# Kernel tuning notes

Measured on AMD Instinct MI355X. Metric: run time of the kernel, lower is better.

The kernel has to match this reference:

```python
import jax, jax.numpy as jnp
import numpy as np

B, S, D = 4, 1024, 1024
H, DH = 16, 64
F = 4 * D
EPS = 1e-6


def _ln(x, scale, bias, axes=-1):
    mean = jnp.mean(x, axis=axes, keepdims=True)
    var = jnp.var(x, axis=axes, keepdims=True)
    return (x - mean) * jax.lax.rsqrt(var + EPS) * scale + bias


def setup_inputs() -> dict:
    key = jax.random.key(0)
    ks = jax.random.split(key, 20)
    sd = 1.0 / np.sqrt(D)
    sf = 1.0 / np.sqrt(F)
    inp = {
        'x': jax.random.normal(ks[0], (B, S, D), jnp.float32),
        'z': jax.random.normal(ks[1], (B, S, D), jnp.float32),
        'ln1_s': jnp.ones((D,), jnp.float32),
        'ln1_b': jnp.zeros((D,), jnp.float32),
        'Wq': jax.random.normal(ks[2], (D, D), jnp.float32) * sd,
        'bq': jnp.zeros((D,), jnp.float32),
        'Wk': jax.random.normal(ks[3], (D, D), jnp.float32) * sd,
        'bk': jnp.zeros((D,), jnp.float32),
        'Wv': jax.random.normal(ks[4], (D, D), jnp.float32) * sd,
        'bv': jnp.zeros((D,), jnp.float32),
        'qn_s': jnp.ones((H, DH), jnp.float32),
        'qn_b': jnp.zeros((H, DH), jnp.float32),
        'kn_s': jnp.ones((H, DH), jnp.float32),
        'kn_b': jnp.zeros((H, DH), jnp.float32),
        'Wo': jax.random.normal(ks[5], (D, D), jnp.float32) * sd,
        'bo': jnp.zeros((D,), jnp.float32),
        'ln2_s': jnp.ones((D,), jnp.float32),
        'ln2_b': jnp.zeros((D,), jnp.float32),
        'W1': jax.random.normal(ks[6], (D, F), jnp.float32) * sd,
        'b1': jnp.zeros((F,), jnp.float32),
        'W2': jax.random.normal(ks[7], (D, F), jnp.float32) * sd,
        'b2': jnp.zeros((F,), jnp.float32),
        'W3': jax.random.normal(ks[8], (F, D), jnp.float32) * sf,
        'b3': jnp.zeros((D,), jnp.float32),
    }
    return inp


def reference(x, z, ln1_s, ln1_b, Wq, bq, Wk, bk, Wv, bv, qn_s, qn_b, kn_s, kn_b,
              Wo, bo, ln2_s, ln2_b, W1, b1, W2, b2, W3, b3):
    # z is unused by the original module body
    x_skip = x
    xn = _ln(x, ln1_s, ln1_b)
    q = (xn @ Wq + bq).reshape(B, S, H, DH)
    k = (xn @ Wk + bk).reshape(B, S, H, DH)
    v = (xn @ Wv + bv).reshape(B, S, H, DH)
    # QK-norm: flax LayerNorm(feature_axes=(-2,-1)) still reduces over axis -1,
    # but carries (H, DH)-shaped scale/bias
    q = _ln(q, qn_s, qn_b)
    k = _ln(k, kn_s, kn_b)
    attn = jnp.einsum('bqhd,bkhd->bhqk', q, k) / jnp.sqrt(jnp.asarray(DH, q.dtype))
    attn = jax.nn.softmax(attn, axis=-1)
    out = jnp.einsum('bhqk,bkhd->bqhd', attn, v).reshape(B, S, D)
    x = x_skip + out @ Wo + bo
    x_skip = x
    xn = _ln(x, ln2_s, ln2_b)
    x1 = xn @ W1 + b1
    x2 = xn @ W2 + b2
    h = x1 * jax.nn.gelu(x2, approximate=True)  # GeGLU
    x = x_skip + h @ W3 + b3
    return x
```

## Files before the change

kernel.cpp:

```cpp
#include <hip/hip_runtime.h>

typedef unsigned short u16;
typedef __bf16  bfrag  __attribute__((ext_vector_type(8)));
typedef float   f32x4  __attribute__((ext_vector_type(4)));
typedef u16     u16x8  __attribute__((ext_vector_type(8)));
typedef u16     u16x4  __attribute__((ext_vector_type(4)));

__device__ __forceinline__ float bf2f(u16 u) {
    unsigned v = ((unsigned)u) << 16;
    return __builtin_bit_cast(float, v);
}
__device__ __forceinline__ u16 f2bf(float f) {
    unsigned x = __builtin_bit_cast(unsigned, f);
    unsigned r = (x + 0x7fffu + ((x >> 16) & 1u)) >> 16;
    return (u16)r;
}
__device__ __forceinline__ void g2l16(const u16* g, u16* l) {
    __builtin_amdgcn_global_load_lds((__attribute__((address_space(1))) void*)g,
                                     (__attribute__((address_space(3))) void*)l, 16, 0, 0);
}
__device__ __forceinline__ float gelu_tanh(float x) {
    float c = 1.5957691216057308f * (x + 0.044715f * x * x * x);
    return x * __frcp_rn(1.0f + __expf(-c));
}

#define SW64(l)   (((((l) & 7) ^ (((l) >> 3) & 7))) * 8)
#define RS64(kk, quad, l15)  (((((kk) * 4 + (quad)) ^ ((l15) & 7))) * 8)

__global__ __launch_bounds__(256) void wtln(
        const float* __restrict__ Wq, const float* __restrict__ Wk,
        const float* __restrict__ Wv, const float* __restrict__ Wo,
        const float* __restrict__ W1, const float* __restrict__ W2,
        const float* __restrict__ W3,
        u16* __restrict__ WqkvT, u16* __restrict__ WoT,
        u16* __restrict__ W12T, u16* __restrict__ W3T,
        const float* __restrict__ x, const float* __restrict__ ln1_s,
        const float* __restrict__ ln1_b, u16* __restrict__ xn1) {
    __shared__ float tile[32][33];
    int blk = blockIdx.x;
    if (blk >= 16384) {
        int row = blk - 16384, t = threadIdx.x;
        float4 v = ((const float4*)(x + (size_t)row * 1024))[t];
        float sum = v.x + v.y + v.z + v.w;
        float sq  = v.x * v.x + v.y * v.y + v.z * v.z + v.w * v.w;
#pragma unroll
        for (int off = 1; off < 64; off <<= 1) {
            sum += __shfl_xor(sum, off);
            sq  += __shfl_xor(sq,  off);
        }
        float* s1 = &tile[0][0];
        float* s2 = &tile[0][8];
        int wave = t >> 6;
        if ((t & 63) == 0) { s1[wave] = sum; s2[wave] = sq; }
        __syncthreads();
        sum = s1[0] + s1[1] + s1[2] + s1[3];
        sq  = s2[0] + s2[1] + s2[2] + s2[3];
        float mean = sum * (1.0f / 1024.0f);
        float var  = sq  * (1.0f / 1024.0f) - mean * mean;
        float inv  = rsqrtf(var + 1e-6f);
        float4 sc = ((const float4*)ln1_s)[t], bb = ((const float4*)ln1_b)[t];
        u16x4 o;
        o[0] = f2bf((v.x - mean) * inv * sc.x + bb.x);
        o[1] = f2bf((v.y - mean) * inv * sc.y + bb.y);
        o[2] = f2bf((v.z - mean) * inv * sc.z + bb.z);
        o[3] = f2bf((v.w - mean) * inv * sc.w + bb.w);
        *(u16x4*)&xn1[(size_t)row * 1024 + t * 4] = o;
        return;
    }
    const float* W; u16* Wt; int R, C, local;
    if (blk < 3072) {
        int w = blk >> 10; local = blk & 1023;
        W = (w == 0) ? Wq : (w == 1) ? Wk : Wv;
        Wt = WqkvT + (size_t)w * 1024 * 1024; R = 1024; C = 1024;
    } else if (blk < 4096) { W = Wo; Wt = WoT; R = 1024; C = 1024; local = blk - 3072; }
    else if (blk < 8192)   { W = W1; Wt = W12T; R = 1024; C = 4096; local = blk - 4096; }
    else if (blk < 12288)  { W = W2; Wt = W12T + (size_t)4096 * 1024; R = 1024; C = 4096; local = blk - 8192; }
    else                   { W = W3; Wt = W3T; R = 4096; C = 1024; local = blk - 12288; }
    int tiles_x = C >> 5;
    int c0 = (local % tiles_x) * 32, r0 = (local / tiles_x) * 32;
    int tx = threadIdx.x & 31, ty = threadIdx.x >> 5;
#pragma unroll
    for (int i = 0; i < 32; i += 8)
        tile[ty + i][tx] = W[(size_t)(r0 + ty + i) * C + c0 + tx];
    __syncthreads();
#pragma unroll
    for (int i = 0; i < 32; i += 8)
        Wt[(size_t)(c0 + ty + i) * R + r0 + tx] = f2bf(tile[tx][ty + i]);
}

template <int EPI>
__global__ __launch_bounds__(256, 3) void gemm64(const u16* __restrict__ A,
                                                 const u16* __restrict__ Bt,
                                                 const float* __restrict__ bias,
                                                 const float* __restrict__ bias2,
                                                 const float* __restrict__ bias3,
                                                 const float* __restrict__ qn_s,
                                                 const float* __restrict__ qn_b,
                                                 const float* __restrict__ kn_s,
                                                 const float* __restrict__ kn_b,
                                                 u16* __restrict__ o0,
                                                 u16* __restrict__ o1,
                                                 u16* __restrict__ o2,
                                                 u16* __restrict__ o3,
                                                 int M, int N, int K, int Klen) {
    __shared__ u16 As[128 * 64];
    __shared__ u16 Bs[128 * 64];
    int tid = threadIdx.x, wave = tid >> 6, lane = tid & 63;
    int quad = lane >> 4, l15 = lane & 15;
    int row0 = blockIdx.y * 128, col0 = blockIdx.x * 128;
    int kz = blockIdx.z;
    int wr = (wave >> 1) * 64, wc = (wave & 1) * 64;
    int swz = SW64(lane);

    f32x4 acc[4][4] = {};

    const u16* gA = A  + (size_t)(row0 + wave * 32 + (lane >> 3)) * K + kz * Klen + swz;
    const u16* gB = Bt + (size_t)(col0 + wave * 32 + (lane >> 3)) * K + kz * Klen + swz;
    u16* lA = &As[wave * 32 * 64];
    u16* lB = &Bs[wave * 32 * 64];

    for (int k0 = 0; k0 < Klen; k0 += 64) {
        __syncthreads();
#pragma unroll
        for (int j = 0; j < 4; j++) {
            g2l16(gA + k0 + j * 8 * K, lA + j * 8 * 64);
            g2l16(gB + k0 + j * 8 * K, lB + j * 8 * 64);
        }
        __syncthreads();
#pragma unroll
        for (int kk = 0; kk < 2; kk++) {
            int rs = RS64(kk, quad, l15);
            bfrag af[4], bf[4];
#pragma unroll
            for (int mi = 0; mi < 4; mi++)
                af[mi] = *(const bfrag*)&As[(wr + mi * 16 + l15) * 64 + rs];
#pragma unroll
            for (int ni = 0; ni < 4; ni++)
                bf[ni] = *(const bfrag*)&Bs[(wc + ni * 16 + l15) * 64 + rs];
#pragma unroll
            for (int mi = 0; mi < 4; mi++)
#pragma unroll
                for (int ni = 0; ni < 4; ni++)
                    acc[mi][ni] = __builtin_amdgcn_mfma_f32_16x16x32_bf16(
                        af[mi], bf[ni], acc[mi][ni], 0, 0, 0);
        }
    }

    if (EPI == 0) {
        u16* P = (kz == 0) ? o0 : (kz == 1) ? o1 : (kz == 2) ? o2 : o3;
#pragma unroll
        for (int mi = 0; mi < 4; mi++) {
            int rbase = row0 + wr + mi * 16 + quad * 4;
#pragma unroll
            for (int r = 0; r < 4; r++)
#pragma unroll
                for (int ni = 0; ni < 4; ni++)
                    P[(size_t)(rbase + r) * N + col0 + wc + ni * 16 + l15] =
                        f2bf(acc[mi][ni][r]);
        }
    } else {
        int cbase = col0 + wc;
        int z = cbase >> 10;
        int hd = (cbase >> 6) & 15;
        const float* bp = (z == 0) ? bias : (z == 1) ? bias2 : bias3;
        float post = (z == 0) ? 0.125f : 1.0f;
        float bv[4], sn[4], bn[4];
#pragma unroll
        for (int ni = 0; ni < 4; ni++)
            bv[ni] = bp[(cbase & 1023) + ni * 16 + l15];
        if (z < 2) {
            const float* ns = (z == 0) ? qn_s : kn_s;
            const float* nb = (z == 0) ? qn_b : kn_b;
#pragma unroll
            for (int ni = 0; ni < 4; ni++) {
                sn[ni] = ns[hd * 64 + ni * 16 + l15];
                bn[ni] = nb[hd * 64 + ni * 16 + l15];
            }
        }
#pragma unroll
        for (int mi = 0; mi < 4; mi++) {
            int rbase = row0 + wr + mi * 16 + quad * 4;
#pragma unroll
            for (int r = 0; r < 4; r++) {
                float v0 = acc[mi][0][r] + bv[0];
                float v1 = acc[mi][1][r] + bv[1];
                float v2 = acc[mi][2][r] + bv[2];
                float v3 = acc[mi][3][r] + bv[3];
                size_t rb = (size_t)(rbase + r) * N + cbase;
                if (z == 2) {
                    o0[rb + 0 * 16 + l15] = f2bf(v0);
                    o0[rb + 1 * 16 + l15] = f2bf(v1);
                    o0[rb + 2 * 16 + l15] = f2bf(v2);
                    o0[rb + 3 * 16 + l15] = f2bf(v3);
                } else {
                    float s  = v0 + v1 + v2 + v3;
                    float sq = v0 * v0 + v1 * v1 + v2 * v2 + v3 * v3;
#pragma unroll
                    for (int m = 1; m < 16; m <<= 1) {
                        s  += __shfl_xor(s,  m);
                        sq += __shfl_xor(sq, m);
                    }
                    float mean = s * (1.0f / 64.0f);
                    float var  = sq * (1.0f / 64.0f) - mean * mean;
                    float inv  = rsqrtf(var + 1e-6f);
                    o0[rb + 0 * 16 + l15] = f2bf(((v0 - mean) * inv * sn[0] + bn[0]) * post);
                    o0[rb + 1 * 16 + l15] = f2bf(((v1 - mean) * inv * sn[1] + bn[1]) * post);
                    o0[rb + 2 * 16 + l15] = f2bf(((v2 - mean) * inv * sn[2] + bn[2]) * post);
                    o0[rb + 3 * 16 + l15] = f2bf(((v3 - mean) * inv * sn[3] + bn[3]) * post);
                }
            }
        }
    }
}

__global__ __launch_bounds__(256, 2) void gemm_w12(const u16* __restrict__ A,
                                                   const u16* __restrict__ W12T,
                                                   const float* __restrict__ b1,
                                                   const float* __restrict__ b2,
                                                   u16* __restrict__ H) {
    __shared__ u16 As[128 * 64];
    __shared__ u16 B1s[128 * 64];
    __shared__ u16 B2s[128 * 64];
    int tid = threadIdx.x, wave = tid >> 6, lane = tid & 63;
    int quad = lane >> 4, l15 = lane & 15;
    int row0 = blockIdx.y * 128, col0 = blockIdx.x * 128;
    int wr = (wave >> 1) * 64, wc = (wave & 1) * 64;
    int swz = SW64(lane);

    f32x4 acc1[4][4] = {}, acc2[4][4] = {};

    const u16* gA  = A    + (size_t)(row0 + wave * 32 + (lane >> 3)) * 1024 + swz;
    const u16* gB1 = W12T + (size_t)(col0 + wave * 32 + (lane >> 3)) * 1024 + swz;
    const u16* gB2 = gB1  + (size_t)4096 * 1024;
    u16* lA  = &As [wave * 32 * 64];
    u16* lB1 = &B1s[wave * 32 * 64];
    u16* lB2 = &B2s[wave * 32 * 64];

    for (int k0 = 0; k0 < 1024; k0 += 64) {
        __syncthreads();
#pragma unroll
        for (int j = 0; j < 4; j++) {
            g2l16(gA  + k0 + j * 8 * 1024, lA  + j * 8 * 64);
            g2l16(gB1 + k0 + j * 8 * 1024, lB1 + j * 8 * 64);
            g2l16(gB2 + k0 + j * 8 * 1024, lB2 + j * 8 * 64);
        }
        __syncthreads();
#pragma unroll
        for (int kk = 0; kk < 2; kk++) {
            int rs = RS64(kk, quad, l15);
            bfrag af[4], b1f[4], b2f[4];
#pragma unroll
            for (int mi = 0; mi < 4; mi++)
                af[mi] = *(const bfrag*)&As[(wr + mi * 16 + l15) * 64 + rs];
#pragma unroll
            for (int ni = 0; ni < 4; ni++) {
                b1f[ni] = *(const bfrag*)&B1s[(wc + ni * 16 + l15) * 64 + rs];
                b2f[ni] = *(const bfrag*)&B2s[(wc + ni * 16 + l15) * 64 + rs];
            }
#pragma unroll
            for (int mi = 0; mi < 4; mi++)
#pragma unroll
                for (int ni = 0; ni < 4; ni++) {
                    acc1[mi][ni] = __builtin_amdgcn_mfma_f32_16x16x32_bf16(
                        af[mi], b1f[ni], acc1[mi][ni], 0, 0, 0);
                    acc2[mi][ni] = __builtin_amdgcn_mfma_f32_16x16x32_bf16(
                        af[mi], b2f[ni], acc2[mi][ni], 0, 0, 0);
                }
        }
    }

    float bv1[4], bv2[4];
    int cols[4];
#pragma unroll
    for (int ni = 0; ni < 4; ni++) {
        cols[ni] = col0 + wc + ni * 16 + l15;
        bv1[ni] = b1[cols[ni]];
        bv2[ni] = b2[cols[ni]];
    }
#pragma unroll
    for (int mi = 0; mi < 4; mi++) {
        int rbase = row0 + wr + mi * 16 + quad * 4;
#pragma unroll
        for (int r = 0; r < 4; r++) {
#pragma unroll
            for (int ni = 0; ni < 4; ni++) {
                float x1 = acc1[mi][ni][r] + bv1[ni];
                float x2 = acc2[mi][ni][r] + bv2[ni];
                H[(size_t)(rbase + r) * 4096 + cols[ni]] = f2bf(x1 * gelu_tanh(x2));
            }
        }
    }
}

__global__ __launch_bounds__(256) void reduce_ln(const u16* __restrict__ p0,
                                                 const u16* __restrict__ p1,
                                                 const float* __restrict__ x,
                                                 const float* __restrict__ bo,
                                                 const float* __restrict__ s,
                                                 const float* __restrict__ b,
                                                 float* __restrict__ xmid,
                                                 u16* __restrict__ xn2) {
    int row = blockIdx.x, t = threadIdx.x;
    size_t i = (size_t)row * 1024 + t * 4;
    float4 xv = *(const float4*)&x[i];
    float4 bb = *(const float4*)&bo[t * 4];
    u16x4 a0 = *(const u16x4*)&p0[i];
    u16x4 a1 = *(const u16x4*)&p1[i];
    float4 v;
    v.x = xv.x + bb.x + bf2f(a0[0]) + bf2f(a1[0]);
    v.y = xv.y + bb.y + bf2f(a0[1]) + bf2f(a1[1]);
    v.z = xv.z + bb.z + bf2f(a0[2]) + bf2f(a1[2]);
    v.w = xv.w + bb.w + bf2f(a0[3]) + bf2f(a1[3]);
    *(float4*)&xmid[i] = v;
    float sum = v.x + v.y + v.z + v.w;
    float sq  = v.x * v.x + v.y * v.y + v.z * v.z + v.w * v.w;
#pragma unroll
    for (int off = 1; off < 64; off <<= 1) {
        sum += __shfl_xor(sum, off);
        sq  += __shfl_xor(sq,  off);
    }
    __shared__ float s1[4], s2[4];
    int wave = t >> 6;
    if ((t & 63) == 0) { s1[wave] = sum; s2[wave] = sq; }
    __syncthreads();
    sum = s1[0] + s1[1] + s1[2] + s1[3];
    sq  = s2[0] + s2[1] + s2[2] + s2[3];
    float mean = sum * (1.0f / 1024.0f);
    float var  = sq  * (1.0f / 1024.0f) - mean * mean;
    float inv  = rsqrtf(var + 1e-6f);
    float4 sc = ((const float4*)s)[t], lb = ((const float4*)b)[t];
    u16x4 o;
    o[0] = f2bf((v.x - mean) * inv * sc.x + lb.x);
    o[1] = f2bf((v.y - mean) * inv * sc.y + lb.y);
    o[2] = f2bf((v.z - mean) * inv * sc.z + lb.z);
    o[3] = f2bf((v.w - mean) * inv * sc.w + lb.w);
    *(u16x4*)&xn2[i] = o;
}

__global__ __launch_bounds__(256) void reduce4(const u16* __restrict__ p0,
                                               const u16* __restrict__ p1,
                                               const u16* __restrict__ p2,
                                               const u16* __restrict__ p3,
                                               const float* __restrict__ xmid,
                                               const float* __restrict__ b3,
                                               float* __restrict__ out) {
    size_t i = ((size_t)blockIdx.x * 256 + threadIdx.x) * 4;
    float4 xm = *(const float4*)&xmid[i];
    float4 bb = *(const float4*)&b3[i & 1023];
    u16x4 a0 = *(const u16x4*)&p0[i];
    u16x4 a1 = *(const u16x4*)&p1[i];
    u16x4 a2 = *(const u16x4*)&p2[i];
    u16x4 a3 = *(const u16x4*)&p3[i];
    float4 o;
    o.x = xm.x + bb.x + bf2f(a0[0]) + bf2f(a1[0]) + bf2f(a2[0]) + bf2f(a3[0]);
    o.y = xm.y + bb.y + bf2f(a0[1]) + bf2f(a1[1]) + bf2f(a2[1]) + bf2f(a3[1]);
    o.z = xm.z + bb.z + bf2f(a0[2]) + bf2f(a1[2]) + bf2f(a2[2]) + bf2f(a3[2]);
    o.w = xm.w + bb.w + bf2f(a0[3]) + bf2f(a1[3]) + bf2f(a2[3]) + bf2f(a3[3]);
    *(float4*)&out[i] = o;
}

#define LPK 72
#define LPV 72
#define LPP 68
__global__ __launch_bounds__(256, 4) void flash(const u16* __restrict__ qkv,
                                                u16* __restrict__ o) {
    int qt = blockIdx.x, h = blockIdx.y, b = blockIdx.z;
    int tid = threadIdx.x, wave = tid >> 6, lane = tid & 63;
    int quad = lane >> 4, l15 = lane & 15;

    __shared__ u16 Ks[64 * LPK];
    __shared__ u16 Vt[64 * LPV];
    __shared__ u16 Ps[64 * LPP];

    const u16* qrow = qkv + (size_t)(b * 1024 + qt * 64 + wave * 16 + l15) * 3072
                      + h * 64 + quad * 8;
    bfrag aq0 = *(const bfrag*)qrow;
    bfrag aq1 = *(const bfrag*)(qrow + 32);

    f32x4 accO[4] = {};
    float l_run[4] = {0.f, 0.f, 0.f, 0.f};

    for (int kt = 0; kt < 16; kt++) {
        __syncthreads();
        {
            int row = tid >> 2, seg = tid & 3;
            const u16* ksrc = qkv + (size_t)(b * 1024 + kt * 64 + row) * 3072
                              + 1024 + h * 64 + seg * 16;
            *(u16x8*)&Ks[row * LPK + seg * 16]     = *(const u16x8*)ksrc;
            *(u16x8*)&Ks[row * LPK + seg * 16 + 8] = *(const u16x8*)(ksrc + 8);
        }
        {
            const u16* vsrc = qkv + (size_t)(b * 1024 + kt * 64 + lane) * 3072
                              + 2048 + h * 64 + wave * 16;
            u16x8 v0 = *(const u16x8*)vsrc, v1 = *(const u16x8*)(vsrc + 8);
#pragma unroll
            for (int j = 0; j < 8; j++) Vt[(wave * 16 + j) * LPV + lane]     = v0[j];
#pragma unroll
            for (int j = 0; j < 8; j++) Vt[(wave * 16 + 8 + j) * LPV + lane] = v1[j];
        }
        __syncthreads();

        f32x4 accS[4] = {};
#pragma unroll
        for (int ct = 0; ct < 4; ct++) {
            bfrag bk0 = *(const bfrag*)&Ks[(ct * 16 + l15) * LPK + quad * 8];
            bfrag bk1 = *(const bfrag*)&Ks[(ct * 16 + l15) * LPK + 32 + quad * 8];
            accS[ct] = __builtin_amdgcn_mfma_f32_16x16x32_bf16(aq0, bk0, accS[ct], 0, 0, 0);
            accS[ct] = __builtin_amdgcn_mfma_f32_16x16x32_bf16(aq1, bk1, accS[ct], 0, 0, 0);
        }

#pragma unroll
        for (int r = 0; r < 4; r++) {
            float p0 = __expf(accS[0][r]);
            float p1 = __expf(accS[1][r]);
            float p2 = __expf(accS[2][r]);
            float p3 = __expf(accS[3][r]);
            l_run[r] += (p0 + p1) + (p2 + p3);
            int pbase = (wave * 16 + quad * 4 + r) * LPP + l15;
            Ps[pbase + 0]  = f2bf(p0);
            Ps[pbase + 16] = f2bf(p1);
            Ps[pbase + 32] = f2bf(p2);
            Ps[pbase + 48] = f2bf(p3);
        }

#pragma unroll
        for (int kk = 0; kk < 2; kk++) {
            const u16* pp = &Ps[(wave * 16 + l15) * LPP + kk * 32 + quad * 8];
            u16x4 lo = *(const u16x4*)pp;
            u16x4 hi = *(const u16x4*)(pp + 4);
            u16x8 apu;
            apu[0] = lo[0]; apu[1] = lo[1]; apu[2] = lo[2]; apu[3] = lo[3];
            apu[4] = hi[0]; apu[5] = hi[1]; apu[6] = hi[2]; apu[7] = hi[3];
            bfrag ap = __builtin_bit_cast(bfrag, apu);
#pragma unroll
            for (int oc = 0; oc < 4; oc++) {
                bfrag bv = *(const bfrag*)&Vt[(oc * 16 + l15) * LPV + kk * 32 + quad * 8];
                accO[oc] = __builtin_amdgcn_mfma_f32_16x16x32_bf16(ap, bv, accO[oc], 0, 0, 0);
            }
        }
    }

#pragma unroll
    for (int r = 0; r < 4; r++) {
        float l = l_run[r];
#pragma unroll
        for (int m = 1; m < 16; m <<= 1) l += __shfl_xor(l, m);
        float linv = 1.0f / l;
        int srow = qt * 64 + wave * 16 + quad * 4 + r;
#pragma unroll
        for (int oc = 0; oc < 4; oc++)
            o[(size_t)(b * 1024 + srow) * 1024 + h * 64 + oc * 16 + l15] =
                f2bf(accO[oc][r] * linv);
    }
}

extern "C" void kernel_launch(void* const* d_in, const int* in_sizes, int n_in,
                              void* d_out, int out_size, void* d_ws, size_t ws_size,
                              hipStream_t stream) {
    const float* x     = (const float*)d_in[0];
    const float* ln1_s = (const float*)d_in[2];
    const float* ln1_b = (const float*)d_in[3];
    const float* Wq = (const float*)d_in[4];  const float* bq = (const float*)d_in[5];
    const float* Wk = (const float*)d_in[6];  const float* bk = (const float*)d_in[7];
    const float* Wv = (const float*)d_in[8];  const float* bv = (const float*)d_in[9];
    const float* qn_s = (const float*)d_in[10]; const float* qn_b = (const float*)d_in[11];
    const float* kn_s = (const float*)d_in[12]; const float* kn_b = (const float*)d_in[13];
    const float* Wo = (const float*)d_in[14]; const float* bo = (const float*)d_in[15];
    const float* ln2_s = (const float*)d_in[16]; const float* ln2_b = (const float*)d_in[17];
    const float* W1 = (const float*)d_in[18]; const float* b1 = (const float*)d_in[19];
    const float* W2 = (const float*)d_in[20]; const float* b2 = (const float*)d_in[21];
    const float* W3 = (const float*)d_in[22]; const float* b3 = (const float*)d_in[23];
    float* out = (float*)d_out;

    char* ws = (char*)d_ws;
    const size_t MB = (size_t)1 << 20;
    u16* WqkvT = (u16*)(ws + 0);
    u16* WoT   = (u16*)(ws + 6 * MB);
    u16* W12T  = (u16*)(ws + 8 * MB);
    u16* W3T   = (u16*)(ws + 24 * MB);
    u16* xn1   = (u16*)(ws + 32 * MB);
    u16* attn  = (u16*)(ws + 32 * MB);
    u16* xn2   = (u16*)(ws + 32 * MB);
    u16* qkv   = (u16*)(ws + 40 * MB);
    float* xmid = (float*)(ws + 40 * MB);
    u16* p3    = (u16*)(ws + 56 * MB);
    u16* h     = (u16*)(ws + 64 * MB);
    u16* wp0   = (u16*)(ws + 64 * MB);
    u16* wp1   = (u16*)(ws + 72 * MB);
    u16* p0    = (u16*)(ws + 0);
    u16* p1    = (u16*)(ws + 8 * MB);
    u16* p2    = (u16*)(ws + 16 * MB);

    wtln<<<20480, 256, 0, stream>>>(Wq, Wk, Wv, Wo, W1, W2, W3,
                                    WqkvT, WoT, W12T, W3T,
                                    x, ln1_s, ln1_b, xn1);

    gemm64<4><<<dim3(24, 32, 1), 256, 0, stream>>>(
        xn1, WqkvT, bq, bk, bv, qn_s, qn_b, kn_s, kn_b,
        qkv, nullptr, nullptr, nullptr, 4096, 3072, 1024, 1024);

    flash<<<dim3(16, 16, 4), 256, 0, stream>>>(qkv, attn);

    gemm64<0><<<dim3(8, 32, 2), 256, 0, stream>>>(
        attn, WoT, nullptr, nullptr, nullptr, nullptr, nullptr, nullptr, nullptr,
        wp0, wp1, nullptr, nullptr, 4096, 1024, 1024, 512);

    reduce_ln<<<4096, 256, 0, stream>>>(wp0, wp1, x, bo, ln2_s, ln2_b, xmid, xn2);

    gemm_w12<<<dim3(32, 32), 256, 0, stream>>>(xn2, W12T, b1, b2, h);

    gemm64<0><<<dim3(8, 32, 4), 256, 0, stream>>>(
        h, W3T, nullptr, nullptr, nullptr, nullptr, nullptr, nullptr, nullptr,
        p0, p1, p2, p3, 4096, 1024, 4096, 1024);

    reduce4<<<4096, 256, 0, stream>>>(p0, p1, p2, p3, xmid, b3, out);
}
```

Measured before the change: 404.7 us.

## Rewrite GeGLU W1/W2 GEMM as 256x256 8-wave double-buffered pipelined kernel

Weight transpose now interleaves W1 and W2 columns in 64-wide groups so one B tile holds matching x1/x2 columns. The GeGLU GEMM becomes a 512-thread kernel with 256x256 tiles and a two-buffer LDS pipeline in 128KB of dynamic shared memory. Its eight phases per K step each overlap global-to-LDS loads with MFMA work, using explicit barriers, vmcnt waits and setprio. The epilogue passes gelu values between paired waves through LDS to form x1*gelu(x2). This trades higher LDS use and lower occupancy for better data reuse and overlap, and relies on hand-written waitcnt logic that must stay correct.

```diff
diff --git a/kernel.cpp b/kernel.cpp
--- a/kernel.cpp
+++ b/kernel.cpp
@@ -67,14 +67,14 @@
         *(u16x4*)&xn1[(size_t)row * 1024 + t * 4] = o;
         return;
     }
-    const float* W; u16* Wt; int R, C, local;
+    const float* W; u16* Wt; int R, C, local; int ilv = -1;
     if (blk < 3072) {
         int w = blk >> 10; local = blk & 1023;
         W = (w == 0) ? Wq : (w == 1) ? Wk : Wv;
         Wt = WqkvT + (size_t)w * 1024 * 1024; R = 1024; C = 1024;
     } else if (blk < 4096) { W = Wo; Wt = WoT; R = 1024; C = 1024; local = blk - 3072; }
-    else if (blk < 8192)   { W = W1; Wt = W12T; R = 1024; C = 4096; local = blk - 4096; }
-    else if (blk < 12288)  { W = W2; Wt = W12T + (size_t)4096 * 1024; R = 1024; C = 4096; local = blk - 8192; }
+    else if (blk < 8192)   { W = W1; Wt = W12T; R = 1024; C = 4096; local = blk - 4096; ilv = 0; }
+    else if (blk < 12288)  { W = W2; Wt = W12T; R = 1024; C = 4096; local = blk - 8192; ilv = 1; }
     else                   { W = W3; Wt = W3T; R = 4096; C = 1024; local = blk - 12288; }
     int tiles_x = C >> 5;
     int c0 = (local % tiles_x) * 32, r0 = (local / tiles_x) * 32;
@@ -84,8 +84,11 @@
         tile[ty + i][tx] = W[(size_t)(r0 + ty + i) * C + c0 + tx];
     __syncthreads();
 #pragma unroll
-    for (int i = 0; i < 32; i += 8)
-        Wt[(size_t)(c0 + ty + i) * R + r0 + tx] = f2bf(tile[tx][ty + i]);
+    for (int i = 0; i < 32; i += 8) {
+        int c = c0 + ty + i;
+        int orow = (ilv < 0) ? c : ((c >> 6) * 128 + ilv * 64 + (c & 63));
+        Wt[(size_t)orow * R + r0 + tx] = f2bf(tile[tx][ty + i]);
+    }
 }
 
 template <int EPI>
@@ -213,80 +216,123 @@
     }
 }
 
-__global__ __launch_bounds__(256, 2) void gemm_w12(const u16* __restrict__ A,
-                                                   const u16* __restrict__ W12T,
-                                                   const float* __restrict__ b1,
-                                                   const float* __restrict__ b2,
-                                                   u16* __restrict__ H) {
-    __shared__ u16 As[128 * 64];
-    __shared__ u16 B1s[128 * 64];
-    __shared__ u16 B2s[128 * 64];
-    int tid = threadIdx.x, wave = tid >> 6, lane = tid & 63;
+#define PH8(BUFI, S, ISSUE, TAIL)                                              \
+  {                                                                            \
+    const u16* LA = sm + (BUFI) * 32768;                                       \
+    const u16* LB = LA + 16384;                                                \
+    if ((S) == 0) {                                                            \
+      _Pragma("unroll") for (int ni = 0; ni < 4; ++ni)                         \
+      _Pragma("unroll") for (int kk = 0; kk < 2; ++kk)                         \
+        bfr[ni][kk] = *(const bfrag*)&LB[(wcg + ni * 16 + l15) * 64            \
+                                         + RS64(kk, quad, l15)];               \
+    }                                                                          \
+    bfrag a00 = *(const bfrag*)&LA[(wr128 + ((S)*2)     * 16 + l15) * 64 + RS64(0, quad, l15)]; \
+    bfrag a01 = *(const bfrag*)&LA[(wr128 + ((S)*2)     * 16 + l15) * 64 + RS64(1, quad, l15)]; \
+    bfrag a10 = *(const bfrag*)&LA[(wr128 + ((S)*2 + 1) * 16 + l15) * 64 + RS64(0, quad, l15)]; \
+    bfrag a11 = *(const bfrag*)&LA[(wr128 + ((S)*2 + 1) * 16 + l15) * 64 + RS64(1, quad, l15)]; \
+    ISSUE;                                                                     \
+    asm volatile("" ::: "memory");                                             \
+    __builtin_amdgcn_s_barrier();                                              \
+    asm volatile("s_waitcnt lgkmcnt(0)" ::: "memory");                         \
+    __builtin_amdgcn_s_setprio(1);                                             \
+    _Pragma("unroll") for (int ni = 0; ni < 4; ++ni) {                         \
+      acc[(S)*2][ni]     = __builtin_amdgcn_mfma_f32_16x16x32_bf16(a00, bfr[ni][0], acc[(S)*2][ni], 0, 0, 0);         \
+      acc[(S)*2][ni]     = __builtin_amdgcn_mfma_f32_16x16x32_bf16(a01, bfr[ni][1], acc[(S)*2][ni], 0, 0, 0);         \
+      acc[(S)*2 + 1][ni] = __builtin_amdgcn_mfma_f32_16x16x32_bf16(a10, bfr[ni][0], acc[(S)*2 + 1][ni], 0, 0, 0);     \
+      acc[(S)*2 + 1][ni] = __builtin_amdgcn_mfma_f32_16x16x32_bf16(a11, bfr[ni][1], acc[(S)*2 + 1][ni], 0, 0, 0);     \
+    }                                                                          \
+    __builtin_amdgcn_s_setprio(0);                                             \
+    TAIL;                                                                      \
+    asm volatile("" ::: "memory");                                             \
+    __builtin_amdgcn_s_barrier();                                              \
+    asm volatile("" ::: "memory");                                             \
+  }
+
+__global__ __launch_bounds__(512, 2) void gemm_w12_8ph(
+        const u16* __restrict__ A, const u16* __restrict__ BI,
+        const float* __restrict__ b1, const float* __restrict__ b2,
+        u16* __restrict__ H) {
+    extern __shared__ __align__(16) u16 sm[];
+    int tid = threadIdx.x, w = tid >> 6, lane = tid & 63;
     int quad = lane >> 4, l15 = lane & 15;
-    int row0 = blockIdx.y * 128, col0 = blockIdx.x * 128;
-    int wr = (wave >> 1) * 64, wc = (wave & 1) * 64;
-    int swz = SW64(lane);
-
-    f32x4 acc1[4][4] = {}, acc2[4][4] = {};
-
-    const u16* gA  = A    + (size_t)(row0 + wave * 32 + (lane >> 3)) * 1024 + swz;
-    const u16* gB1 = W12T + (size_t)(col0 + wave * 32 + (lane >> 3)) * 1024 + swz;
-    const u16* gB2 = gB1  + (size_t)4096 * 1024;
-    u16* lA  = &As [wave * 32 * 64];
-    u16* lB1 = &B1s[wave * 32 * 64];
-    u16* lB2 = &B2s[wave * 32 * 64];
-
-    for (int k0 = 0; k0 < 1024; k0 += 64) {
-        __syncthreads();
-#pragma unroll
-        for (int j = 0; j < 4; j++) {
-            g2l16(gA  + k0 + j * 8 * 1024, lA  + j * 8 * 64);
-            g2l16(gB1 + k0 + j * 8 * 1024, lB1 + j * 8 * 64);
-            g2l16(gB2 + k0 + j * 8 * 1024, lB2 + j * 8 * 64);
-        }
-        __syncthreads();
-#pragma unroll
-        for (int kk = 0; kk < 2; kk++) {
-            int rs = RS64(kk, quad, l15);
-            bfrag af[4], b1f[4], b2f[4];
-#pragma unroll
-            for (int mi = 0; mi < 4; mi++)
-                af[mi] = *(const bfrag*)&As[(wr + mi * 16 + l15) * 64 + rs];
-#pragma unroll
-            for (int ni = 0; ni < 4; ni++) {
-                b1f[ni] = *(const bfrag*)&B1s[(wc + ni * 16 + l15) * 64 + rs];
-                b2f[ni] = *(const bfrag*)&B2s[(wc + ni * 16 + l15) * 64 + rs];
-            }
-#pragma unroll
-            for (int mi = 0; mi < 4; mi++)
-#pragma unroll
-                for (int ni = 0; ni < 4; ni++) {
-                    acc1[mi][ni] = __builtin_amdgcn_mfma_f32_16x16x32_bf16(
-                        af[mi], b1f[ni], acc1[mi][ni], 0, 0, 0);
-                    acc2[mi][ni] = __builtin_amdgcn_mfma_f32_16x16x32_bf16(
-                        af[mi], b2f[ni], acc2[mi][ni], 0, 0, 0);
-                }
-        }
-    }
-
-    float bv1[4], bv2[4];
-    int cols[4];
-#pragma unroll
-    for (int ni = 0; ni < 4; ni++) {
-        cols[ni] = col0 + wc + ni * 16 + l15;
-        bv1[ni] = b1[cols[ni]];
-        bv2[ni] = b2[cols[ni]];
-    }
-#pragma unroll
-    for (int mi = 0; mi < 4; mi++) {
-        int rbase = row0 + wr + mi * 16 + quad * 4;
-#pragma unroll
-        for (int r = 0; r < 4; r++) {
-#pragma unroll
-            for (int ni = 0; ni < 4; ni++) {
-                float x1 = acc1[mi][ni][r] + bv1[ni];
-                float x2 = acc2[mi][ni][r] + bv2[ni];
-                H[(size_t)(rbase + r) * 4096 + cols[ni]] = f2bf(x1 * gelu_tanh(x2));
+    int row0  = blockIdx.y * 256;
+    int nrow0 = blockIdx.x * 256;
+    int wr128 = (w >> 2) * 128, wcg = (w & 3) * 64;
+    int strow = w * 8 + (lane >> 3);
+    int swz8  = ((lane & 7) ^ ((lane >> 3) & 7)) * 8;
+    int lw8   = w * 8;
+
+    const u16* gA = A  + (size_t)(row0  + strow) * 1024 + swz8;
+    const u16* gB = BI + (size_t)(nrow0 + strow) * 1024 + swz8;
+
+    f32x4 acc[8][4] = {};
+    bfrag bfr[4][2];
+
+    auto stage = [&](int bufi, int isB, int half, int t) {
+        const u16* g = (isB ? gB : gA) + (size_t)half * 128 * 1024 + t * 64;
+        u16* l = sm + bufi * 32768 + isB * 16384 + (half * 128 + lw8) * 64;
+        g2l16(g, l);
+        g2l16(g + 64 * 1024, l + 64 * 64);
+    };
+
+    stage(0, 1, 0, 0); stage(0, 1, 1, 0);
+    stage(0, 0, 0, 0); stage(0, 0, 1, 0);
+    stage(1, 1, 0, 1); stage(1, 1, 1, 1);
+    asm volatile("s_waitcnt vmcnt(4)" ::: "memory");
+    __builtin_amdgcn_s_barrier();
+    asm volatile("" ::: "memory");
+
+#pragma unroll 1
+    for (int i = 0; i < 8; ++i) {
+        int t = 2 * i;
+        bool more = (i < 7);
+        PH8(0, 0, { stage(1, 0, 0, t + 1); }, {});
+        PH8(0, 1, { stage(1, 0, 1, t + 1); }, {});
+        PH8(0, 2, { if (more) stage(0, 1, 0, t + 2); }, {});
+        PH8(0, 3, { if (more) stage(0, 1, 1, t + 2); },
+                  { if (more) asm volatile("s_waitcnt vmcnt(4)" ::: "memory");
+                    else      asm volatile("s_waitcnt vmcnt(0)" ::: "memory"); });
+        PH8(1, 0, { if (more) stage(0, 0, 0, t + 2); }, {});
+        PH8(1, 1, { if (more) stage(0, 0, 1, t + 2); }, {});
+        PH8(1, 2, { if (more) stage(1, 1, 0, t + 3); }, {});
+        PH8(1, 3, { if (more) stage(1, 1, 1, t + 3); },
+                  { if (more) asm volatile("s_waitcnt vmcnt(4)" ::: "memory"); });
+    }
+
+    int c0 = blockIdx.x * 128 + ((w & 3) >> 1) * 64;
+    const float* bp = (w & 1) ? b2 : b1;
+    float bvv[4];
+#pragma unroll
+    for (int ni = 0; ni < 4; ++ni) bvv[ni] = bp[c0 + ni * 16 + l15];
+
+    float* xg = (float*)(void*)sm + (w >> 1) * (128 * 64);
+    if (w & 1) {
+#pragma unroll
+        for (int mi = 0; mi < 8; ++mi)
+#pragma unroll
+        for (int ni = 0; ni < 4; ++ni) {
+            int lc = (ni * 16 + l15) ^ (quad << 4);
+#pragma unroll
+            for (int r = 0; r < 4; ++r)
+                xg[(mi * 16 + quad * 4 + r) * 64 + lc] =
+                    gelu_tanh(acc[mi][ni][r] + bvv[ni]);
+        }
+    }
+    asm volatile("" ::: "memory");
+    __builtin_amdgcn_s_barrier();
+    asm volatile("" ::: "memory");
+    if (!(w & 1)) {
+#pragma unroll
+        for (int mi = 0; mi < 8; ++mi) {
+            int gr = row0 + wr128 + mi * 16 + quad * 4;
+#pragma unroll
+            for (int r = 0; r < 4; ++r)
+#pragma unroll
+            for (int ni = 0; ni < 4; ++ni) {
+                float g = xg[(mi * 16 + quad * 4 + r) * 64
+                             + ((ni * 16 + l15) ^ (quad << 4))];
+                H[(size_t)(gr + r) * 4096 + c0 + ni * 16 + l15] =
+                    f2bf((acc[mi][ni][r] + bvv[ni]) * g);
             }
         }
     }
@@ -507,7 +553,7 @@
 
     reduce_ln<<<4096, 256, 0, stream>>>(wp0, wp1, x, bo, ln2_s, ln2_b, xmid, xn2);
 
-    gemm_w12<<<dim3(32, 32), 256, 0, stream>>>(xn2, W12T, b1, b2, h);
+    gemm_w12_8ph<<<dim3(32, 16), 512, 131072, stream>>>(xn2, W12T, b1, b2, h);
 
     gemm64<0><<<dim3(8, 32, 4), 256, 0, stream>>>(
         h, W3T, nullptr, nullptr, nullptr, nullptr, nullptr, nullptr, nullptr,
```

Measured after the change: 417.6 us. +3.2%, slower.

## Double-buffer LDS and enlarge W12 GEMM tile to 256 rows with 512 threads

Applied to the files above, without the earlier changes.

The GeGLU W1/W2 GEMM now uses a 256x128 output tile computed by 8 waves per block. Operand staging moves to a dynamic 128KB LDS double buffer, so the async global-to-LDS loads for the next K step are issued before the MFMA work on the current one. This leaves one barrier per iteration instead of two. The aim is to hide global load latency and reuse each B tile across more rows, at the cost of fewer resident blocks per CU because of the large LDS footprint.

```diff
diff --git a/kernel.cpp b/kernel.cpp
--- a/kernel.cpp
+++ b/kernel.cpp
@@ -213,49 +213,58 @@
     }
 }
 
-__global__ __launch_bounds__(256, 2) void gemm_w12(const u16* __restrict__ A,
+__global__ __launch_bounds__(512, 2) void gemm_w12(const u16* __restrict__ A,
                                                    const u16* __restrict__ W12T,
                                                    const float* __restrict__ b1,
                                                    const float* __restrict__ b2,
                                                    u16* __restrict__ H) {
-    __shared__ u16 As[128 * 64];
-    __shared__ u16 B1s[128 * 64];
-    __shared__ u16 B2s[128 * 64];
-    int tid = threadIdx.x, wave = tid >> 6, lane = tid & 63;
+    extern __shared__ __align__(16) u16 sm[];
+    int tid = threadIdx.x, w = tid >> 6, lane = tid & 63;
     int quad = lane >> 4, l15 = lane & 15;
-    int row0 = blockIdx.y * 128, col0 = blockIdx.x * 128;
-    int wr = (wave >> 1) * 64, wc = (wave & 1) * 64;
-    int swz = SW64(lane);
+    int row0 = blockIdx.y * 256, col0 = blockIdx.x * 128;
+    int wr = (w >> 1) * 64, wc = (w & 1) * 64;
+    int swz8 = SW64(lane);
 
     f32x4 acc1[4][4] = {}, acc2[4][4] = {};
 
-    const u16* gA  = A    + (size_t)(row0 + wave * 32 + (lane >> 3)) * 1024 + swz;
-    const u16* gB1 = W12T + (size_t)(col0 + wave * 32 + (lane >> 3)) * 1024 + swz;
+    const u16* gA  = A    + (size_t)(row0 + w * 8 + (lane >> 3)) * 1024 + swz8;
+    const u16* gB1 = W12T + (size_t)(col0 + w * 8 + (lane >> 3)) * 1024 + swz8;
     const u16* gB2 = gB1  + (size_t)4096 * 1024;
-    u16* lA  = &As [wave * 32 * 64];
-    u16* lB1 = &B1s[wave * 32 * 64];
-    u16* lB2 = &B2s[wave * 32 * 64];
-
-    for (int k0 = 0; k0 < 1024; k0 += 64) {
-        __syncthreads();
-#pragma unroll
-        for (int j = 0; j < 4; j++) {
-            g2l16(gA  + k0 + j * 8 * 1024, lA  + j * 8 * 64);
-            g2l16(gB1 + k0 + j * 8 * 1024, lB1 + j * 8 * 64);
-            g2l16(gB2 + k0 + j * 8 * 1024, lB2 + j * 8 * 64);
-        }
-        __syncthreads();
+
+    auto stage = [&](int bufi, int t) {
+        u16* base = sm + bufi * 32768;
+        const u16* ga  = gA  + t * 64;
+        const u16* gb1 = gB1 + t * 64;
+        const u16* gb2 = gB2 + t * 64;
+#pragma unroll
+        for (int j = 0; j < 4; j++)
+            g2l16(ga + (size_t)j * 64 * 1024, base + (j * 64 + w * 8) * 64);
+#pragma unroll
+        for (int j = 0; j < 2; j++) {
+            g2l16(gb1 + (size_t)j * 64 * 1024, base + 16384 + (j * 64 + w * 8) * 64);
+            g2l16(gb2 + (size_t)j * 64 * 1024, base + 24576 + (j * 64 + w * 8) * 64);
+        }
+    };
+
+    stage(0, 0);
+    __syncthreads();
+
+    for (int t = 0; t < 16; ++t) {
+        if (t < 15) stage((t + 1) & 1, t + 1);
+        const u16* lA  = sm + (t & 1) * 32768;
+        const u16* lB1 = lA + 16384;
+        const u16* lB2 = lA + 24576;
 #pragma unroll
         for (int kk = 0; kk < 2; kk++) {
             int rs = RS64(kk, quad, l15);
             bfrag af[4], b1f[4], b2f[4];
 #pragma unroll
             for (int mi = 0; mi < 4; mi++)
-                af[mi] = *(const bfrag*)&As[(wr + mi * 16 + l15) * 64 + rs];
+                af[mi] = *(const bfrag*)&lA[(wr + mi * 16 + l15) * 64 + rs];
 #pragma unroll
             for (int ni = 0; ni < 4; ni++) {
-                b1f[ni] = *(const bfrag*)&B1s[(wc + ni * 16 + l15) * 64 + rs];
-                b2f[ni] = *(const bfrag*)&B2s[(wc + ni * 16 + l15) * 64 + rs];
+                b1f[ni] = *(const bfrag*)&lB1[(wc + ni * 16 + l15) * 64 + rs];
+                b2f[ni] = *(const bfrag*)&lB2[(wc + ni * 16 + l15) * 64 + rs];
             }
 #pragma unroll
             for (int mi = 0; mi < 4; mi++)
@@ -267,6 +276,7 @@
                         af[mi], b2f[ni], acc2[mi][ni], 0, 0, 0);
                 }
         }
+        __syncthreads();
     }
 
     float bv1[4], bv2[4];
@@ -507,7 +517,7 @@
 
     reduce_ln<<<4096, 256, 0, stream>>>(wp0, wp1, x, bo, ln2_s, ln2_b, xmid, xn2);
 
-    gemm_w12<<<dim3(32, 32), 256, 0, stream>>>(xn2, W12T, b1, b2, h);
+    gemm_w12<<<dim3(32, 16), 512, 131072, stream>>>(xn2, W12T, b1, b2, h);
 
     gemm64<0><<<dim3(8, 32, 4), 256, 0, stream>>>(
         h, W3T, nullptr, nullptr, nullptr, nullptr, nullptr, nullptr, nullptr,
```

Result: no change. 398.0 us (-1.7%).
